# Optimization experiments

Hardware: AMD Instinct MI355X
Metric: run time of the kernel (lower is better)

Reference implementation:

```python
import jax, jax.numpy as jnp
import numpy as np

N = 20000      # u/v nodes (dst == src, no block sampling)
E = 200000     # edges per direction
EIN = UIN = VIN = EOUT = 64
UOUT = VOUT = 128
NU = UOUT // 2
NV = VOUT // 2
ATT = VIN + EIN  # 128, W_ATTN output / concat dim


def _linear_params(key, din, dout):
    kw, kb = jax.random.split(key)
    s = 1.0 / np.sqrt(din)
    w = jax.random.uniform(kw, (din, dout), jnp.float32, -s, s)
    b = jax.random.uniform(kb, (dout,), jnp.float32, -s, s)
    return w, b


def setup_inputs() -> dict:
    key = jax.random.key(0)
    ks = jax.random.split(key, 20)
    inp = {
        "f_feat": jax.random.normal(ks[0], (E, EIN), jnp.float32),
        "b_feat": jax.random.normal(ks[1], (E, EIN), jnp.float32),
        "u_feat": jax.random.normal(ks[2], (N, UIN), jnp.float32),
        "v_feat": jax.random.normal(ks[3], (N, VIN), jnp.float32),
        "fw_src": jax.random.randint(ks[4], (E,), 0, N, jnp.int32),
        "fw_dst": jax.random.randint(ks[5], (E,), 0, N, jnp.int32),
        "bw_src": jax.random.randint(ks[6], (E,), 0, N, jnp.int32),
        "bw_dst": jax.random.randint(ks[7], (E,), 0, N, jnp.int32),
    }
    names_dims = [("e", EIN, EOUT), ("u", UIN, EOUT), ("v", VIN, EOUT),
                  ("au", UIN, ATT), ("av", VIN, ATT),
                  ("Wu", ATT, NU), ("Wv", ATT, NV),
                  ("Vu", UIN, UOUT - NU), ("Vv", VIN, VOUT - NV)]
    for i, (nm, di, do) in enumerate(names_dims):
        w, b = _linear_params(ks[8 + i], di, do)
        inp["w_" + nm] = w
        inp["b_" + nm] = b
    return inp


def _seg_softmax(x, seg, n):
    # softmax over edges grouped by destination node, per channel
    m = jax.ops.segment_max(x, seg, num_segments=n)       # [n, d]
    e = jnp.exp(x - m[seg])
    s = jax.ops.segment_sum(e, seg, num_segments=n)       # [n, d]
    return e / s[seg]


def reference(f_feat, b_feat, u_feat, v_feat, fw_src, fw_dst, bw_src, bw_dst,
              w_e, b_e, w_u, b_u, w_v, b_v, w_au, b_au, w_av, b_av,
              w_Wu, b_Wu, w_Wv, b_Wv, w_Vu, b_Vu, w_Vv, b_Vv):
    relu = jax.nn.relu
    src_he_u = u_feat @ w_u + b_u                 # [N, EOUT]
    src_he_v = v_feat @ w_v + b_v                 # [N, EOUT]
    dst_he_u = src_he_u                           # dst slice == full set
    dst_he_v = v_feat @ w_u + b_u                 # faithful: original applies u_linear to dst v feats
    fw_he_e = f_feat @ w_e + b_e                  # [E, EOUT]
    bw_he_e = b_feat @ w_e + b_e
    # edge updates (gather-add-activate)
    hf = relu(bw_he_e + dst_he_u[bw_src] + src_he_v[bw_dst])   # [E, EOUT]
    hb = relu(fw_he_e + src_he_u[fw_src] + dst_he_v[fw_dst])
    # per-edge concat features
    h_ve = jnp.concatenate([v_feat[bw_src], b_feat], -1)       # [E, ATT]
    h_ue = jnp.concatenate([u_feat[fw_src], f_feat], -1)       # [E, ATT]
    # attention scores: elementwise edge * gathered node projection
    h_att_u = u_feat @ w_au + b_au                # [N, ATT]
    h_att_v = v_feat @ w_av + b_av
    bw_edotv = h_ve * h_att_u[bw_src]
    fw_edotv = h_ue * h_att_v[fw_src]
    bw_sfm = _seg_softmax(bw_edotv, bw_dst, N)
    fw_sfm = _seg_softmax(fw_edotv, fw_dst, N)
    # weighted segment-sum aggregation
    agg_u = jax.ops.segment_sum(h_ve * bw_sfm, bw_dst, num_segments=N)  # [N, ATT]
    agg_v = jax.ops.segment_sum(h_ue * fw_sfm, fw_dst, num_segments=N)
    h_nu = relu(agg_u @ w_Wu + b_Wu)              # [N, NU]
    h_nv = relu(agg_v @ w_Wv + b_Wv)
    hu = jnp.concatenate([u_feat @ w_Vu + b_Vu, h_nu], -1)     # [N, UOUT]
    hv = jnp.concatenate([v_feat @ w_Vv + b_Vv, h_nv], -1)     # [N, VOUT]
    return (hf, hb, hu, hv)
```

## Files before the change

### kernel.cpp

```cpp
#include <hip/hip_runtime.h>

#define NNODES 20000
#define NEDGES 200000

__global__ __launch_bounds__(256)
void zero_kernel(float4* __restrict__ p, long n4)
{
    long i = (long)blockIdx.x * 256 + threadIdx.x;
    if (i < n4) p[i] = make_float4(0.f, 0.f, 0.f, 0.f);
}

__global__ __launch_bounds__(256)
void hist2_kernel(const int* __restrict__ dst0, const int* __restrict__ dst1,
                  int* __restrict__ deg0, int* __restrict__ deg1, int n)
{
    const int e = blockIdx.x * 256 + threadIdx.x;
    if (e >= n) return;
    if (blockIdx.y == 0) atomicAdd(&deg0[dst0[e]], 1);
    else                 atomicAdd(&deg1[dst1[e]], 1);
}

__global__ __launch_bounds__(1024)
void scan2_kernel(const int* __restrict__ deg0, const int* __restrict__ deg1,
                  int* __restrict__ rp0, int* __restrict__ rp1,
                  int* __restrict__ cur0, int* __restrict__ cur1, int n)
{
    const int* deg = blockIdx.x == 0 ? deg0 : deg1;
    int* rowptr    = blockIdx.x == 0 ? rp0  : rp1;
    int* cursor    = blockIdx.x == 0 ? cur0 : cur1;

    __shared__ int part[1024];
    const int t  = threadIdx.x;
    const int CH = (n + 1023) / 1024;
    const int base = t * CH;

    int s = 0;
    for (int i = 0; i < CH; ++i) {
        int idx = base + i;
        if (idx < n) s += deg[idx];
    }
    part[t] = s;
    __syncthreads();
    for (int off = 1; off < 1024; off <<= 1) {
        int v = 0;
        if (t >= off) v = part[t - off];
        __syncthreads();
        if (t >= off) part[t] += v;
        __syncthreads();
    }
    int run = (t == 0) ? 0 : part[t - 1];
    for (int i = 0; i < CH; ++i) {
        int idx = base + i;
        if (idx < n) {
            int dv = deg[idx];
            rowptr[idx] = run;
            cursor[idx] = run;
            run += dv;
        }
    }
    if (t == 1023) rowptr[n] = part[1023];
}

__global__ __launch_bounds__(256)
void scatter2_kernel(const int* __restrict__ dst0, const int* __restrict__ dst1,
                     int* __restrict__ cur0, int* __restrict__ cur1,
                     int* __restrict__ ei0, int* __restrict__ ei1, int n)
{
    const int e = blockIdx.x * 256 + threadIdx.x;
    if (e >= n) return;
    if (blockIdx.y == 0) { int p = atomicAdd(&cur0[dst0[e]], 1); ei0[p] = e; }
    else                 { int p = atomicAdd(&cur1[dst1[e]], 1); ei1[p] = e; }
}

__global__ __launch_bounds__(128)
void agg3_kernel(const float* __restrict__ fn0, const float* __restrict__ fe0,
                 const float* __restrict__ ha0, const int* __restrict__ src0,
                 const int* __restrict__ ei0,  const int* __restrict__ rp0,
                 float* __restrict__ agg0,
                 const float* __restrict__ fn1, const float* __restrict__ fe1,
                 const float* __restrict__ ha1, const int* __restrict__ src1,
                 const int* __restrict__ ei1,  const int* __restrict__ rp1,
                 float* __restrict__ agg1)
{
    const int y = blockIdx.y;
    const float* __restrict__ feat_node = y == 0 ? fn0 : fn1;
    const float* __restrict__ feat_edge = y == 0 ? fe0 : fe1;
    const float* __restrict__ h_att     = y == 0 ? ha0 : ha1;
    const int*   __restrict__ src       = y == 0 ? src0 : src1;
    const int*   __restrict__ eidx      = y == 0 ? ei0 : ei1;
    const int*   __restrict__ rowptr    = y == 0 ? rp0 : rp1;
    float*       __restrict__ agg       = y == 0 ? agg0 : agg1;

    const int d = blockIdx.x;
    const int c = threadIdx.x;
    const int lo = rowptr[d], hi = rowptr[d + 1];
    const bool low = c < 64;

    __shared__ int se[64];
    __shared__ int ss[64];

    float ssum = 0.f, anum = 0.f;

    for (int base = lo; base < hi; base += 64) {
        const int cnt = min(64, hi - base);
        if (c < cnt) {
            const int e = eidx[base + c];
            se[c] = e;
            ss[c] = src[e];
        }
        __syncthreads();

        int i = 0;
        for (; i + 4 <= cnt; i += 4) {
            float hv[4], at[4];
            #pragma unroll
            for (int j = 0; j < 4; ++j) {
                const int e = se[i + j];
                const int s = ss[i + j];
                hv[j] = low ? feat_node[(long)s * 64 + c]
                            : feat_edge[(long)e * 64 + (c - 64)];
                at[j] = h_att[(long)s * 128 + c];
            }
            #pragma unroll
            for (int j = 0; j < 4; ++j) {
                const float p = __expf(hv[j] * at[j]);
                ssum += p;
                anum += hv[j] * p;
            }
        }
        for (; i < cnt; ++i) {
            const int e = se[i];
            const int s = ss[i];
            const float hvv = low ? feat_node[(long)s * 64 + c]
                                  : feat_edge[(long)e * 64 + (c - 64)];
            const float att = h_att[(long)s * 128 + c];
            const float p = __expf(hvv * att);
            ssum += p;
            anum += hvv * p;
        }
        __syncthreads();
    }
    agg[(long)d * 128 + c] = (hi > lo) ? anum / ssum : 0.f;
}

struct LinArgs {
    const float* x[5];
    const float* W[5];
    const float* bias[5];
    float*       out[5];
    long         ostride[5];
};

template<int DIN, int DOUT, int BLOCK, bool RELU>
__global__ __launch_bounds__(BLOCK)
void lin_batch_kernel(LinArgs a, int nrows)
{
    constexpr int BR  = 16 * BLOCK / DOUT;
    constexpr int BRP = BR + 4;
    constexpr int KV  = DIN / 4;
    constexpr int JT  = DOUT / 4;

    const int y = blockIdx.y;
    const float* __restrict__ x    = a.x[y];
    const float* __restrict__ W    = a.W[y];
    const float* __restrict__ bias = a.bias[y];
    float* __restrict__ out        = a.out[y];
    const long ostride             = a.ostride[y];

    __shared__ float xs[DIN * BRP];

    const int tid  = threadIdx.x;
    const int row0 = blockIdx.x * BR;

    const int kv = tid % KV;
    for (int rr = tid / KV; rr < BR; rr += BLOCK / KV) {
        const int row = row0 + rr;
        float4 v = make_float4(0.f, 0.f, 0.f, 0.f);
        if (row < nrows)
            v = ((const float4*)x)[(long)row * KV + kv];
        xs[(kv * 4 + 0) * BRP + rr] = v.x;
        xs[(kv * 4 + 1) * BRP + rr] = v.y;
        xs[(kv * 4 + 2) * BRP + rr] = v.z;
        xs[(kv * 4 + 3) * BRP + rr] = v.w;
    }
    __syncthreads();

    const int jt = tid % JT;
    const int rt = tid / JT;

    float4 b4 = ((const float4*)bias)[jt];
    float acc[4][4];
    #pragma unroll
    for (int r = 0; r < 4; ++r) {
        acc[r][0] = b4.x; acc[r][1] = b4.y; acc[r][2] = b4.z; acc[r][3] = b4.w;
    }

    const float4* __restrict__ W4 = (const float4*)W;
    #pragma unroll 4
    for (int k = 0; k < DIN; ++k) {
        float4 w  = W4[k * JT + jt];
        float4 x4 = *((const float4*)(xs + k * BRP + rt * 4));
        float xr[4] = {x4.x, x4.y, x4.z, x4.w};
        #pragma unroll
        for (int r = 0; r < 4; ++r) {
            acc[r][0] = fmaf(xr[r], w.x, acc[r][0]);
            acc[r][1] = fmaf(xr[r], w.y, acc[r][1]);
            acc[r][2] = fmaf(xr[r], w.z, acc[r][2]);
            acc[r][3] = fmaf(xr[r], w.w, acc[r][3]);
        }
    }

    #pragma unroll
    for (int r = 0; r < 4; ++r) {
        const int row = row0 + rt * 4 + r;
        if (row >= nrows) continue;
        float4 o = make_float4(acc[r][0], acc[r][1], acc[r][2], acc[r][3]);
        if (RELU) {
            o.x = fmaxf(o.x, 0.f); o.y = fmaxf(o.y, 0.f);
            o.z = fmaxf(o.z, 0.f); o.w = fmaxf(o.w, 0.f);
        }
        *((float4*)(out + (long)row * ostride) + jt) = o;
    }
}

struct EdgeArgs {
    const float* x[2];
    const float* tabA[2];
    const float* tabB[2];
    const int*   idxA[2];
    const int*   idxB[2];
    float*       out[2];
};

__global__ __launch_bounds__(256)
void edge_batch_kernel(EdgeArgs a, const float* __restrict__ W,
                       const float* __restrict__ bias, int nrows)
{
    constexpr int DIN = 64, DOUT = 64, BLOCK = 256;
    constexpr int BR  = 16 * BLOCK / DOUT;
    constexpr int BRP = BR + 4;
    constexpr int KV  = DIN / 4;
    constexpr int JT  = DOUT / 4;

    const int y = blockIdx.y;
    const float* __restrict__ x    = a.x[y];
    const float* __restrict__ tabA = a.tabA[y];
    const float* __restrict__ tabB = a.tabB[y];
    const int* __restrict__ idxA   = a.idxA[y];
    const int* __restrict__ idxB   = a.idxB[y];
    float* __restrict__ out        = a.out[y];

    __shared__ float xs[DIN * BRP];

    const int tid  = threadIdx.x;
    const int row0 = blockIdx.x * BR;

    const int kv = tid % KV;
    for (int rr = tid / KV; rr < BR; rr += BLOCK / KV) {
        const int row = row0 + rr;
        float4 v = make_float4(0.f, 0.f, 0.f, 0.f);
        if (row < nrows)
            v = ((const float4*)x)[(long)row * KV + kv];
        xs[(kv * 4 + 0) * BRP + rr] = v.x;
        xs[(kv * 4 + 1) * BRP + rr] = v.y;
        xs[(kv * 4 + 2) * BRP + rr] = v.z;
        xs[(kv * 4 + 3) * BRP + rr] = v.w;
    }
    __syncthreads();

    const int jt = tid % JT;
    const int rt = tid / JT;

    float4 b4 = ((const float4*)bias)[jt];
    float acc[4][4];
    #pragma unroll
    for (int r = 0; r < 4; ++r) {
        acc[r][0] = b4.x; acc[r][1] = b4.y; acc[r][2] = b4.z; acc[r][3] = b4.w;
    }

    const float4* __restrict__ W4 = (const float4*)W;
    #pragma unroll 4
    for (int k = 0; k < DIN; ++k) {
        float4 w  = W4[k * JT + jt];
        float4 x4 = *((const float4*)(xs + k * BRP + rt * 4));
        float xr[4] = {x4.x, x4.y, x4.z, x4.w};
        #pragma unroll
        for (int r = 0; r < 4; ++r) {
            acc[r][0] = fmaf(xr[r], w.x, acc[r][0]);
            acc[r][1] = fmaf(xr[r], w.y, acc[r][1]);
            acc[r][2] = fmaf(xr[r], w.z, acc[r][2]);
            acc[r][3] = fmaf(xr[r], w.w, acc[r][3]);
        }
    }

    #pragma unroll
    for (int r = 0; r < 4; ++r) {
        const int row = row0 + rt * 4 + r;
        if (row >= nrows) continue;
        const int ia = idxA[row];
        const int ib = idxB[row];
        float4 ga = ((const float4*)(tabA + (long)ia * DOUT))[jt];
        float4 gb = ((const float4*)(tabB + (long)ib * DOUT))[jt];
        float4 o;
        o.x = fmaxf(acc[r][0] + ga.x + gb.x, 0.f);
        o.y = fmaxf(acc[r][1] + ga.y + gb.y, 0.f);
        o.z = fmaxf(acc[r][2] + ga.z + gb.z, 0.f);
        o.w = fmaxf(acc[r][3] + ga.w + gb.w, 0.f);
        *((float4*)(out + (long)row * DOUT) + jt) = o;
    }
}

extern "C" void kernel_launch(void* const* d_in, const int* in_sizes, int n_in,
                              void* d_out, int out_size, void* d_ws, size_t ws_size,
                              hipStream_t stream)
{
    const float* f_feat = (const float*)d_in[0];
    const float* b_feat = (const float*)d_in[1];
    const float* u_feat = (const float*)d_in[2];
    const float* v_feat = (const float*)d_in[3];
    const int* fw_src = (const int*)d_in[4];
    const int* fw_dst = (const int*)d_in[5];
    const int* bw_src = (const int*)d_in[6];
    const int* bw_dst = (const int*)d_in[7];
    const float* w_e  = (const float*)d_in[8];   const float* b_e  = (const float*)d_in[9];
    const float* w_u  = (const float*)d_in[10];  const float* b_u  = (const float*)d_in[11];
    const float* w_v  = (const float*)d_in[12];  const float* b_v  = (const float*)d_in[13];
    const float* w_au = (const float*)d_in[14];  const float* b_au = (const float*)d_in[15];
    const float* w_av = (const float*)d_in[16];  const float* b_av = (const float*)d_in[17];
    const float* w_Wu = (const float*)d_in[18];  const float* b_Wu = (const float*)d_in[19];
    const float* w_Wv = (const float*)d_in[20];  const float* b_Wv = (const float*)d_in[21];
    const float* w_Vu = (const float*)d_in[22];  const float* b_Vu = (const float*)d_in[23];
    const float* w_Vv = (const float*)d_in[24];  const float* b_Vv = (const float*)d_in[25];

    const int N = NNODES, E = NEDGES;

    float* out = (float*)d_out;
    float* hf = out;
    float* hb = hf + (long)E * 64;
    float* hu = hb + (long)E * 64;
    float* hv = hu + (long)N * 128;

    float* h_att_u = hf;
    float* h_att_v = h_att_u + (long)N * 128;

    float* ws = (float*)d_ws;
    float* src_he_u = ws;
    float* src_he_v = src_he_u + (long)N * 64;
    float* dst_he_v = src_he_v + (long)N * 64;
    float* agg_u    = dst_he_v + (long)N * 64;
    float* agg_v    = agg_u    + (long)N * 128;
    int*   ibase    = (int*)(agg_v + (long)N * 128);
    int* deg_b    = ibase;
    int* deg_f    = deg_b + N;
    int* rowptr_b = deg_f + N;
    int* rowptr_f = rowptr_b + (N + 1);
    int* cursor_b = rowptr_f + (N + 1);
    int* cursor_f = cursor_b + N;
    int* eidx_b   = cursor_f + N;
    int* eidx_f   = eidx_b + E;

    const size_t ws_need = (size_t)((long)8960000 + 520002 + 2) * sizeof(float);
    if (ws_size < ws_need) return;

    zero_kernel<<<dim3((2 * N / 4 + 255) / 256), dim3(256), 0, stream>>>(
        (float4*)deg_b, (long)2 * N / 4);

    const int gN64 = (N + 63) / 64;
    const int gN32 = (N + 31) / 32;
    const int gE64 = (E + 63) / 64;
    const int gE   = (E + 255) / 256;

    hist2_kernel<<<dim3(gE, 2), dim3(256), 0, stream>>>(
        bw_dst, fw_dst, deg_b, deg_f, E);
    scan2_kernel<<<dim3(2), dim3(1024), 0, stream>>>(
        deg_b, deg_f, rowptr_b, rowptr_f, cursor_b, cursor_f, N);
    scatter2_kernel<<<dim3(gE, 2), dim3(256), 0, stream>>>(
        bw_dst, fw_dst, cursor_b, cursor_f, eidx_b, eidx_f, E);

    {
        LinArgs a;
        a.x[0]=u_feat; a.W[0]=w_u;  a.bias[0]=b_u;  a.out[0]=src_he_u; a.ostride[0]=64;
        a.x[1]=v_feat; a.W[1]=w_v;  a.bias[1]=b_v;  a.out[1]=src_he_v; a.ostride[1]=64;
        a.x[2]=v_feat; a.W[2]=w_u;  a.bias[2]=b_u;  a.out[2]=dst_he_v; a.ostride[2]=64;
        a.x[3]=u_feat; a.W[3]=w_Vu; a.bias[3]=b_Vu; a.out[3]=hu;       a.ostride[3]=128;
        a.x[4]=v_feat; a.W[4]=w_Vv; a.bias[4]=b_Vv; a.out[4]=hv;       a.ostride[4]=128;
        lin_batch_kernel<64,64,256,false><<<dim3(gN64, 5), dim3(256), 0, stream>>>(a, N);
    }

    {
        LinArgs a = {};
        a.x[0]=u_feat; a.W[0]=w_au; a.bias[0]=b_au; a.out[0]=h_att_u; a.ostride[0]=128;
        a.x[1]=v_feat; a.W[1]=w_av; a.bias[1]=b_av; a.out[1]=h_att_v; a.ostride[1]=128;
        lin_batch_kernel<64,128,256,false><<<dim3(gN32, 2), dim3(256), 0, stream>>>(a, N);
    }

    agg3_kernel<<<dim3(N, 2), dim3(128), 0, stream>>>(
        v_feat, b_feat, h_att_u, bw_src, eidx_b, rowptr_b, agg_u,
        u_feat, f_feat, h_att_v, fw_src, eidx_f, rowptr_f, agg_v);

    {
        LinArgs a = {};
        a.x[0]=agg_u; a.W[0]=w_Wu; a.bias[0]=b_Wu; a.out[0]=hu + 64; a.ostride[0]=128;
        a.x[1]=agg_v; a.W[1]=w_Wv; a.bias[1]=b_Wv; a.out[1]=hv + 64; a.ostride[1]=128;
        lin_batch_kernel<128,64,128,true><<<dim3(gN32, 2), dim3(128), 0, stream>>>(a, N);
    }

    {
        EdgeArgs a;
        a.x[0]=b_feat; a.tabA[0]=src_he_u; a.tabB[0]=src_he_v;
        a.idxA[0]=bw_src; a.idxB[0]=bw_dst; a.out[0]=hf;
        a.x[1]=f_feat; a.tabA[1]=src_he_u; a.tabB[1]=dst_he_v;
        a.idxA[1]=fw_src; a.idxB[1]=fw_dst; a.out[1]=hb;
        edge_batch_kernel<<<dim3(gE64, 2), dim3(256), 0, stream>>>(a, w_e, b_e, E);
    }
}
```

Measured before the change: 480.3 us.

## Use 8x8 register-tiled GEMM with shared-memory weights for node and edge linears

Adds lin8 and edge8 kernels in which each thread computes an 8x8 output tile instead of 4x4, with the weight matrix staged in padded shared memory and the input rows stored as interleaved float4 so each load is reused. The edge kernel also loads all gather indices before doing the gathers. The small linear kernel with DIN=128 changes its shared-memory padding to BR+1 and reads scalars. The aim is higher arithmetic intensity and fewer global weight reads per FMA, at the cost of more registers and lower occupancy.

```diff
diff --git a/kernel.cpp b/kernel.cpp
--- a/kernel.cpp
+++ b/kernel.cpp
@@ -151,12 +151,223 @@
     long         ostride[5];
 };
 
+template<int DOUT, bool RELU>
+__global__ __launch_bounds__(128)
+void lin8_kernel(LinArgs a, int nrows)
+{
+    constexpr int BLOCK = 128;
+    constexpr int DIN = 64;
+    constexpr int KV  = DIN / 4;
+    constexpr int JT  = DOUT / 8;
+    constexpr int RT  = BLOCK / JT;
+    constexpr int BR  = RT * 8;
+    constexpr int BQ  = BR / 4;
+    constexpr int XSTR = BR + 1;
+    constexpr int WSTR = DOUT + 4;
+
+    const int y = blockIdx.y;
+    const float* __restrict__ x    = a.x[y];
+    const float* __restrict__ W    = a.W[y];
+    const float* __restrict__ bias = a.bias[y];
+    float* __restrict__ out        = a.out[y];
+    const long ostride             = a.ostride[y];
+
+    __shared__ float4 xs4[KV * XSTR];
+    __shared__ float  Ws[DIN * WSTR];
+
+    const int tid  = threadIdx.x;
+    const int row0 = blockIdx.x * BR;
+
+    const float4* __restrict__ W4 = (const float4*)W;
+    for (int i = tid; i < DIN * DOUT / 4; i += BLOCK) {
+        const int k = i / (DOUT / 4), c4 = i % (DOUT / 4);
+        ((float4*)(Ws + k * WSTR))[(c4 & 1) * JT + (c4 >> 1)] = W4[i];
+    }
+    const float4* __restrict__ X4 = (const float4*)x;
+    for (int i = tid; i < BR * KV; i += BLOCK) {
+        const int rr = i >> 4, kv = i & 15;
+        const int row = row0 + rr;
+        float4 v = make_float4(0.f, 0.f, 0.f, 0.f);
+        if (row < nrows) v = X4[(long)row * KV + kv];
+        xs4[kv * XSTR + (rr & 3) * BQ + (rr >> 2)] = v;
+    }
+    __syncthreads();
+
+    const int jt = tid % JT;
+    const int rt = tid / JT;
+
+    float4 b0 = ((const float4*)bias)[jt * 2];
+    float4 b1 = ((const float4*)bias)[jt * 2 + 1];
+    float acc[8][8];
+    #pragma unroll
+    for (int r = 0; r < 8; ++r) {
+        acc[r][0] = b0.x; acc[r][1] = b0.y; acc[r][2] = b0.z; acc[r][3] = b0.w;
+        acc[r][4] = b1.x; acc[r][5] = b1.y; acc[r][6] = b1.z; acc[r][7] = b1.w;
+    }
+
+    #pragma unroll 2
+    for (int kv = 0; kv < KV; ++kv) {
+        float4 xq[8];
+        #pragma unroll
+        for (int r = 0; r < 8; ++r)
+            xq[r] = xs4[kv * XSTR + (r & 3) * BQ + rt * 2 + (r >> 2)];
+        #pragma unroll
+        for (int q = 0; q < 4; ++q) {
+            const int k = kv * 4 + q;
+            float4 wa = ((const float4*)(Ws + k * WSTR))[jt];
+            float4 wb = ((const float4*)(Ws + k * WSTR))[JT + jt];
+            const float wc[8] = {wa.x, wa.y, wa.z, wa.w, wb.x, wb.y, wb.z, wb.w};
+            #pragma unroll
+            for (int r = 0; r < 8; ++r) {
+                const float xk = q == 0 ? xq[r].x : q == 1 ? xq[r].y
+                               : q == 2 ? xq[r].z : xq[r].w;
+                #pragma unroll
+                for (int c = 0; c < 8; ++c)
+                    acc[r][c] = fmaf(xk, wc[c], acc[r][c]);
+            }
+        }
+    }
+
+    #pragma unroll
+    for (int r = 0; r < 8; ++r) {
+        const int row = row0 + rt * 8 + r;
+        if (row >= nrows) continue;
+        float4 o0 = make_float4(acc[r][0], acc[r][1], acc[r][2], acc[r][3]);
+        float4 o1 = make_float4(acc[r][4], acc[r][5], acc[r][6], acc[r][7]);
+        if (RELU) {
+            o0.x = fmaxf(o0.x, 0.f); o0.y = fmaxf(o0.y, 0.f);
+            o0.z = fmaxf(o0.z, 0.f); o0.w = fmaxf(o0.w, 0.f);
+            o1.x = fmaxf(o1.x, 0.f); o1.y = fmaxf(o1.y, 0.f);
+            o1.z = fmaxf(o1.z, 0.f); o1.w = fmaxf(o1.w, 0.f);
+        }
+        float4* op = (float4*)(out + (long)row * ostride);
+        op[jt * 2]     = o0;
+        op[jt * 2 + 1] = o1;
+    }
+}
+
+struct EdgeArgs {
+    const float* x[2];
+    const float* tabA[2];
+    const float* tabB[2];
+    const int*   idxA[2];
+    const int*   idxB[2];
+    float*       out[2];
+};
+
+__global__ __launch_bounds__(128)
+void edge8_kernel(EdgeArgs a, const float* __restrict__ W,
+                  const float* __restrict__ bias, int nrows)
+{
+    constexpr int BLOCK = 128;
+    constexpr int DIN = 64, DOUT = 64;
+    constexpr int KV  = 16;
+    constexpr int JT  = 8;
+    constexpr int BR  = 128;
+    constexpr int BQ  = 32;
+    constexpr int XSTR = BR + 1;
+    constexpr int WSTR = DOUT + 4;
+
+    const int y = blockIdx.y;
+    const float* __restrict__ x    = a.x[y];
+    const float* __restrict__ tabA = a.tabA[y];
+    const float* __restrict__ tabB = a.tabB[y];
+    const int* __restrict__ idxA   = a.idxA[y];
+    const int* __restrict__ idxB   = a.idxB[y];
+    float* __restrict__ out        = a.out[y];
+
+    __shared__ float4 xs4[KV * XSTR];
+    __shared__ float  Ws[DIN * WSTR];
+
+    const int tid  = threadIdx.x;
+    const int row0 = blockIdx.x * BR;
+
+    const float4* __restrict__ W4 = (const float4*)W;
+    for (int i = tid; i < DIN * DOUT / 4; i += BLOCK) {
+        const int k = i / (DOUT / 4), c4 = i % (DOUT / 4);
+        ((float4*)(Ws + k * WSTR))[(c4 & 1) * JT + (c4 >> 1)] = W4[i];
+    }
+    const float4* __restrict__ X4 = (const float4*)x;
+    for (int i = tid; i < BR * KV; i += BLOCK) {
+        const int rr = i >> 4, kv = i & 15;
+        const int row = row0 + rr;
+        float4 v = make_float4(0.f, 0.f, 0.f, 0.f);
+        if (row < nrows) v = X4[(long)row * KV + kv];
+        xs4[kv * XSTR + (rr & 3) * BQ + (rr >> 2)] = v;
+    }
+    __syncthreads();
+
+    const int jt = tid % JT;
+    const int rt = tid / JT;
+
+    float4 b0 = ((const float4*)bias)[jt * 2];
+    float4 b1 = ((const float4*)bias)[jt * 2 + 1];
+    float acc[8][8];
+    #pragma unroll
+    for (int r = 0; r < 8; ++r) {
+        acc[r][0] = b0.x; acc[r][1] = b0.y; acc[r][2] = b0.z; acc[r][3] = b0.w;
+        acc[r][4] = b1.x; acc[r][5] = b1.y; acc[r][6] = b1.z; acc[r][7] = b1.w;
+    }
+
+    #pragma unroll 2
+    for (int kv = 0; kv < KV; ++kv) {
+        float4 xq[8];
+        #pragma unroll
+        for (int r = 0; r < 8; ++r)
+            xq[r] = xs4[kv * XSTR + (r & 3) * BQ + rt * 2 + (r >> 2)];
+        #pragma unroll
+        for (int q = 0; q < 4; ++q) {
+            const int k = kv * 4 + q;
+            float4 wa = ((const float4*)(Ws + k * WSTR))[jt];
+            float4 wb = ((const float4*)(Ws + k * WSTR))[JT + jt];
+            const float wc[8] = {wa.x, wa.y, wa.z, wa.w, wb.x, wb.y, wb.z, wb.w};
+            #pragma unroll
+            for (int r = 0; r < 8; ++r) {
+                const float xk = q == 0 ? xq[r].x : q == 1 ? xq[r].y
+                               : q == 2 ? xq[r].z : xq[r].w;
+                #pragma unroll
+                for (int c = 0; c < 8; ++c)
+                    acc[r][c] = fmaf(xk, wc[c], acc[r][c]);
+            }
+        }
+    }
+
+    int ia[8], ib[8];
+    #pragma unroll
+    for (int r = 0; r < 8; ++r) {
+        const int row = row0 + rt * 8 + r;
+        ia[r] = (row < nrows) ? idxA[row] : 0;
+        ib[r] = (row < nrows) ? idxB[row] : 0;
+    }
+    #pragma unroll
+    for (int r = 0; r < 8; ++r) {
+        const int row = row0 + rt * 8 + r;
+        if (row >= nrows) continue;
+        const float4* tA = (const float4*)(tabA + (long)ia[r] * 64);
+        const float4* tB = (const float4*)(tabB + (long)ib[r] * 64);
+        float4 ga0 = tA[jt * 2], ga1 = tA[jt * 2 + 1];
+        float4 gb0 = tB[jt * 2], gb1 = tB[jt * 2 + 1];
+        float4 o0, o1;
+        o0.x = fmaxf(acc[r][0] + ga0.x + gb0.x, 0.f);
+        o0.y = fmaxf(acc[r][1] + ga0.y + gb0.y, 0.f);
+        o0.z = fmaxf(acc[r][2] + ga0.z + gb0.z, 0.f);
+        o0.w = fmaxf(acc[r][3] + ga0.w + gb0.w, 0.f);
+        o1.x = fmaxf(acc[r][4] + ga1.x + gb1.x, 0.f);
+        o1.y = fmaxf(acc[r][5] + ga1.y + gb1.y, 0.f);
+        o1.z = fmaxf(acc[r][6] + ga1.z + gb1.z, 0.f);
+        o1.w = fmaxf(acc[r][7] + ga1.w + gb1.w, 0.f);
+        float4* op = (float4*)(out + (long)row * 64);
+        op[jt * 2]     = o0;
+        op[jt * 2 + 1] = o1;
+    }
+}
+
 template<int DIN, int DOUT, int BLOCK, bool RELU>
 __global__ __launch_bounds__(BLOCK)
-void lin_batch_kernel(LinArgs a, int nrows)
+void lin_small_kernel(LinArgs a, int nrows)
 {
     constexpr int BR  = 16 * BLOCK / DOUT;
-    constexpr int BRP = BR + 4;
+    constexpr int BRP = BR + 1;
     constexpr int KV  = DIN / 4;
     constexpr int JT  = DOUT / 4;
 
@@ -198,9 +409,10 @@
     const float4* __restrict__ W4 = (const float4*)W;
     #pragma unroll 4
     for (int k = 0; k < DIN; ++k) {
-        float4 w  = W4[k * JT + jt];
-        float4 x4 = *((const float4*)(xs + k * BRP + rt * 4));
-        float xr[4] = {x4.x, x4.y, x4.z, x4.w};
+        float4 w = W4[k * JT + jt];
+        float xr[4];
+        #pragma unroll
+        for (int r = 0; r < 4; ++r) xr[r] = xs[k * BRP + rt * 4 + r];
         #pragma unroll
         for (int r = 0; r < 4; ++r) {
             acc[r][0] = fmaf(xr[r], w.x, acc[r][0]);
@@ -220,93 +432,6 @@
             o.z = fmaxf(o.z, 0.f); o.w = fmaxf(o.w, 0.f);
         }
         *((float4*)(out + (long)row * ostride) + jt) = o;
-    }
-}
-
-struct EdgeArgs {
-    const float* x[2];
-    const float* tabA[2];
-    const float* tabB[2];
-    const int*   idxA[2];
-    const int*   idxB[2];
-    float*       out[2];
-};
-
-__global__ __launch_bounds__(256)
-void edge_batch_kernel(EdgeArgs a, const float* __restrict__ W,
-                       const float* __restrict__ bias, int nrows)
-{
-    constexpr int DIN = 64, DOUT = 64, BLOCK = 256;
-    constexpr int BR  = 16 * BLOCK / DOUT;
-    constexpr int BRP = BR + 4;
-    constexpr int KV  = DIN / 4;
-    constexpr int JT  = DOUT / 4;
-
-    const int y = blockIdx.y;
-    const float* __restrict__ x    = a.x[y];
-    const float* __restrict__ tabA = a.tabA[y];
-    const float* __restrict__ tabB = a.tabB[y];
-    const int* __restrict__ idxA   = a.idxA[y];
-    const int* __restrict__ idxB   = a.idxB[y];
-    float* __restrict__ out        = a.out[y];
-
-    __shared__ float xs[DIN * BRP];
-
-    const int tid  = threadIdx.x;
-    const int row0 = blockIdx.x * BR;
-
-    const int kv = tid % KV;
-    for (int rr = tid / KV; rr < BR; rr += BLOCK / KV) {
-        const int row = row0 + rr;
-        float4 v = make_float4(0.f, 0.f, 0.f, 0.f);
-        if (row < nrows)
-            v = ((const float4*)x)[(long)row * KV + kv];
-        xs[(kv * 4 + 0) * BRP + rr] = v.x;
-        xs[(kv * 4 + 1) * BRP + rr] = v.y;
-        xs[(kv * 4 + 2) * BRP + rr] = v.z;
-        xs[(kv * 4 + 3) * BRP + rr] = v.w;
-    }
-    __syncthreads();
-
-    const int jt = tid % JT;
-    const int rt = tid / JT;
-
-    float4 b4 = ((const float4*)bias)[jt];
-    float acc[4][4];
-    #pragma unroll
-    for (int r = 0; r < 4; ++r) {
-        acc[r][0] = b4.x; acc[r][1] = b4.y; acc[r][2] = b4.z; acc[r][3] = b4.w;
-    }
-
-    const float4* __restrict__ W4 = (const float4*)W;
-    #pragma unroll 4
-    for (int k = 0; k < DIN; ++k) {
-        float4 w  = W4[k * JT + jt];
-        float4 x4 = *((const float4*)(xs + k * BRP + rt * 4));
-        float xr[4] = {x4.x, x4.y, x4.z, x4.w};
-        #pragma unroll
-        for (int r = 0; r < 4; ++r) {
-            acc[r][0] = fmaf(xr[r], w.x, acc[r][0]);
-            acc[r][1] = fmaf(xr[r], w.y, acc[r][1]);
-            acc[r][2] = fmaf(xr[r], w.z, acc[r][2]);
-            acc[r][3] = fmaf(xr[r], w.w, acc[r][3]);
-        }
-    }
-
-    #pragma unroll
-    for (int r = 0; r < 4; ++r) {
-        const int row = row0 + rt * 4 + r;
-        if (row >= nrows) continue;
-        const int ia = idxA[row];
-        const int ib = idxB[row];
-        float4 ga = ((const float4*)(tabA + (long)ia * DOUT))[jt];
-        float4 gb = ((const float4*)(tabB + (long)ib * DOUT))[jt];
-        float4 o;
-        o.x = fmaxf(acc[r][0] + ga.x + gb.x, 0.f);
-        o.y = fmaxf(acc[r][1] + ga.y + gb.y, 0.f);
-        o.z = fmaxf(acc[r][2] + ga.z + gb.z, 0.f);
-        o.w = fmaxf(acc[r][3] + ga.w + gb.w, 0.f);
-        *((float4*)(out + (long)row * DOUT) + jt) = o;
     }
 }
 
@@ -365,10 +490,7 @@
     zero_kernel<<<dim3((2 * N / 4 + 255) / 256), dim3(256), 0, stream>>>(
         (float4*)deg_b, (long)2 * N / 4);
 
-    const int gN64 = (N + 63) / 64;
-    const int gN32 = (N + 31) / 32;
-    const int gE64 = (E + 63) / 64;
-    const int gE   = (E + 255) / 256;
+    const int gE = (E + 255) / 256;
 
     hist2_kernel<<<dim3(gE, 2), dim3(256), 0, stream>>>(
         bw_dst, fw_dst, deg_b, deg_f, E);
@@ -384,14 +506,14 @@
         a.x[2]=v_feat; a.W[2]=w_u;  a.bias[2]=b_u;  a.out[2]=dst_he_v; a.ostride[2]=64;
         a.x[3]=u_feat; a.W[3]=w_Vu; a.bias[3]=b_Vu; a.out[3]=hu;       a.ostride[3]=128;
         a.x[4]=v_feat; a.W[4]=w_Vv; a.bias[4]=b_Vv; a.out[4]=hv;       a.ostride[4]=128;
-        lin_batch_kernel<64,64,256,false><<<dim3(gN64, 5), dim3(256), 0, stream>>>(a, N);
+        lin8_kernel<64,false><<<dim3((N + 127) / 128, 5), dim3(128), 0, stream>>>(a, N);
     }
 
     {
         LinArgs a = {};
         a.x[0]=u_feat; a.W[0]=w_au; a.bias[0]=b_au; a.out[0]=h_att_u; a.ostride[0]=128;
         a.x[1]=v_feat; a.W[1]=w_av; a.bias[1]=b_av; a.out[1]=h_att_v; a.ostride[1]=128;
-        lin_batch_kernel<64,128,256,false><<<dim3(gN32, 2), dim3(256), 0, stream>>>(a, N);
+        lin8_kernel<128,false><<<dim3((N + 63) / 64, 2), dim3(128), 0, stream>>>(a, N);
     }
 
     agg3_kernel<<<dim3(N, 2), dim3(128), 0, stream>>>(
@@ -402,7 +524,7 @@
         LinArgs a = {};
         a.x[0]=agg_u; a.W[0]=w_Wu; a.bias[0]=b_Wu; a.out[0]=hu + 64; a.ostride[0]=128;
         a.x[1]=agg_v; a.W[1]=w_Wv; a.bias[1]=b_Wv; a.out[1]=hv + 64; a.ostride[1]=128;
-        lin_batch_kernel<128,64,128,true><<<dim3(gN32, 2), dim3(128), 0, stream>>>(a, N);
+        lin_small_kernel<128,64,128,true><<<dim3((N + 31) / 32, 2), dim3(128), 0, stream>>>(a, N);
     }
 
     {
@@ -411,6 +533,6 @@
         a.idxA[0]=bw_src; a.idxB[0]=bw_dst; a.out[0]=hf;
         a.x[1]=f_feat; a.tabA[1]=src_he_u; a.tabB[1]=dst_he_v;
         a.idxA[1]=fw_src; a.idxB[1]=fw_dst; a.out[1]=hb;
-        edge_batch_kernel<<<dim3(gE64, 2), dim3(256), 0, stream>>>(a, w_e, b_e, E);
-    }
-}
+        edge8_kernel<<<dim3((E + 127) / 128, 2), dim3(128), 0, stream>>>(a, w_e, b_e, E);
+    }
+}
```

New measurement: 522.5 us. +8.8%, slower.
